# Performance work log

Hardware: AMD Instinct MI355X
Metric: run time of the kernel (lower is better)

The kernel has to match this reference:

```python
import jax, jax.numpy as jnp
import numpy as np
from jax import lax

COCO_80_TO_91 = [1,2,3,4,5,6,7,8,9,10,11,13,14,15,16,17,18,19,20,21,22,23,24,25,27,28,31,32,33,34,35,36,37,38,39,40,41,42,43,44,46,47,48,49,50,51,52,53,54,55,56,57,58,59,60,61,62,63,64,65,67,70,72,73,74,75,76,77,78,79,80,81,82,84,85,86,87,88,89,90]

CONF = 0.25      # self.confidence
IOU_THR = 0.7    # ultralytics NMS default
TOPK = 1000      # candidate cap before NMS
MAX_DET = 300    # ultralytics max_det default
MAX_WH = 7680.0  # per-class offset trick
IMG_SZ = 640.0   # yolov8 letterboxed input size


def setup_inputs() -> dict:
    key = jax.random.key(0)
    preds = jax.random.uniform(key, (32, 84, 8400), dtype=jnp.float32)
    return {"preds": preds}


def _nms_single(boxes, scores):
    """Greedy NMS on score-descending boxes [K,4] (class-offset xyxy). Returns keep mask [K]."""
    K = boxes.shape[0]
    area = (boxes[:, 2] - boxes[:, 0]) * (boxes[:, 3] - boxes[:, 1])  # [K]
    lt = jnp.maximum(boxes[:, None, :2], boxes[None, :, :2])          # [K,K,2]
    rb = jnp.minimum(boxes[:, None, 2:], boxes[None, :, 2:])
    wh = jnp.clip(rb - lt, 0.0)
    inter = wh[..., 0] * wh[..., 1]
    iou = inter / (area[:, None] + area[None, :] - inter + 1e-7)       # [K,K]
    idx = jnp.arange(K)
    sup = (iou > IOU_THR) & (idx[None, :] > idx[:, None])              # i suppresses later j

    def body(i, keep):
        return jnp.where(keep[i], keep & ~sup[i], keep)

    return lax.fori_loop(0, K, body, jnp.ones((K,), dtype=bool))


def reference(preds):
    # preds: [B, 84, N] -> [B, N, 84]
    p = jnp.transpose(preds, (0, 2, 1))
    box_xywh = p[..., :4] * IMG_SZ           # xywh in pixels on 640x640 canvas
    cls = p[..., 4:]                          # [B, N, 80]
    scores = jnp.max(cls, axis=-1)            # best-class confidence
    labels = jnp.argmax(cls, axis=-1)         # 0..79
    xy, wh = box_xywh[..., :2], box_xywh[..., 2:]
    xyxy = jnp.concatenate([xy - wh * 0.5, xy + wh * 0.5], axis=-1)  # decode

    # confidence filter + top-K candidate selection (score-descending)
    s_masked = jnp.where(scores > CONF, scores, -1.0)
    top_s, top_i = lax.top_k(s_masked, TOPK)                          # [B,TOPK]
    top_b = jnp.take_along_axis(xyxy, top_i[..., None], axis=1)      # [B,TOPK,4]
    top_l = jnp.take_along_axis(labels, top_i, axis=1)               # [B,TOPK]

    # per-class NMS via class offset
    off_b = top_b + (top_l.astype(top_b.dtype) * MAX_WH)[..., None]
    keep = jax.vmap(_nms_single)(off_b, top_s) & (top_s > CONF)

    # select final max_det detections, zero-pad invalid slots
    fin_s = jnp.where(keep, top_s, -1.0)
    out_s, out_i = lax.top_k(fin_s, MAX_DET)                          # [B,MAX_DET]
    out_b = jnp.take_along_axis(top_b, out_i[..., None], axis=1)
    out_l = jnp.take_along_axis(top_l, out_i, axis=1)
    valid = out_s > CONF
    boxes = jnp.where(valid[..., None], out_b, 0.0)
    scores_out = jnp.where(valid, out_s, 0.0)
    mapped = jnp.asarray(COCO_80_TO_91, dtype=jnp.int64)[out_l]       # COCO 80 -> 91 ids
    labels_out = jnp.where(valid, mapped, 0)
    return boxes, scores_out, labels_out
```

## Files before the change

kernel.cpp:

```cpp
#include <hip/hip_runtime.h>
#include <stdint.h>

typedef unsigned long long u64;
typedef unsigned int u32;

#define BATCH 32
#define NCH 84
#define NA 8400
#define NCLS 80
#define TOPK 1000
#define MAXDET 300
#define CONF 0.25f
#define IOU_T 0.7f
#define MAX_WH 7680.0f
#define IMG_SZ 640.0f
#define NT 1024
#define KPT 9
#define NCOPY 8
#define HPAD 260

__device__ __constant__ float coco_map_f[NCLS] = {
    1,2,3,4,5,6,7,8,9,10,11,13,14,15,16,17,18,19,20,21,22,23,24,25,27,28,
    31,32,33,34,35,36,37,38,39,40,41,42,43,44,46,47,48,49,50,51,52,53,54,
    55,56,57,58,59,60,61,62,63,64,65,67,70,72,73,74,75,76,77,78,79,80,81,
    82,84,85,86,87,88,89,90};

__device__ inline u64 shflx64(u64 v, int m) {
    int lo = __shfl_xor((int)(u32)(v & 0xFFFFFFFFull), m, 64);
    int hi = __shfl_xor((int)(u32)(v >> 32), m, 64);
    return ((u64)(u32)hi << 32) | (u32)lo;
}

__global__ __launch_bounds__(256)
void decode_kernel(const float* __restrict__ preds,
                   u64* __restrict__ keys,
                   float4* __restrict__ boxes) {
    const int b = blockIdx.y;
    const int a = blockIdx.x * 256 + threadIdx.x;
    const bool live = (a < NA);
    const int ac = live ? a : (NA - 1);
    const float* p = preds + (size_t)b * NCH * NA + ac;

    float bx = p[0];
    float by = p[(size_t)1 * NA];
    float bw = p[(size_t)2 * NA];
    float bh = p[(size_t)3 * NA];

    const float* pc = p + (size_t)4 * NA;
    float best = -1.0f;
    int bl = 0;
#pragma unroll 16
    for (int r = 0; r < NCLS; ++r) {
        float v = pc[(size_t)r * NA];
        bl = (v > best) ? r : bl;
        best = fmaxf(v, best);
    }

    if (live) {
        float fx = bx * IMG_SZ, fy = by * IMG_SZ;
        float fw = bw * IMG_SZ, fh = bh * IMG_SZ;
        float hw = fw * 0.5f, hh = fh * 0.5f;
        boxes[(size_t)b * NA + a] = make_float4(fx - hw, fy - hh, fx + hw, fy + hh);
        float s = (best > CONF) ? best : -1.0f;
        u32 fb = __float_as_uint(s);
        u32 u = (fb & 0x80000000u) ? ~fb : (fb | 0x80000000u);
        keys[(size_t)b * NA + a] =
            ((u64)u << 21) | ((u64)(16383 - a) << 7) | (u64)bl;
    }
}

__global__ __launch_bounds__(NT, 4)
void select_sort_kernel(const u64* __restrict__ keys,
                        const float4* __restrict__ boxes,
                        u64* __restrict__ sortedk,
                        float4* __restrict__ gbox,
                        float4* __restrict__ goffb,
                        float* __restrict__ garea,
                        unsigned short* __restrict__ grank,
                        int* __restrict__ gccnt) {
    const int b = blockIdx.x;
    const int t = threadIdx.x;
    const int lane = t & 63, wid = t >> 6;

    __shared__ union {
        struct {
            u64 sk[2][NT];
            int hist[NCOPY * HPAD];
        } a;
        struct {
            u64 cmask2[NCLS][16];
        } bb;
    } u_s;
    __shared__ int selB, selK, hselS, cnt_s;
    __shared__ int wsum[16], woff[16];

    u64 kreg[KPT];
    const u64* kb = keys + (size_t)b * NA;
#pragma unroll
    for (int j = 0; j < KPT; ++j) {
        int i = t + j * NT;
        kreg[j] = (i < NA) ? kb[i] : 0ull;
    }

    u64 P = 0ull;
    int kk = TOPK;
    int nsel = 0;
    bool done = false;
    bool did16 = false;

    {
        int dg[KPT];
        int mymax = -1;
#pragma unroll
        for (int j = 0; j < KPT; ++j) {
            dg[j] = (kreg[j] != 0ull) ? (int)((kreg[j] >> 37) & 0xFFFF) : -1;
            mymax = max(mymax, dg[j]);
        }
#pragma unroll
        for (int off = 32; off; off >>= 1)
            mymax = max(mymax, __shfl_down(mymax, off, 64));
        if (lane == 0) wsum[wid] = mymax;
        __syncthreads();
        int maxd = wsum[0];
#pragma unroll
        for (int q = 1; q < 16; ++q) maxd = max(maxd, wsum[q]);
        int myc = 0;
#pragma unroll
        for (int j = 0; j < KPT; ++j) myc += (dg[j] == maxd) ? 1 : 0;
#pragma unroll
        for (int off = 32; off; off >>= 1) myc += __shfl_down(myc, off, 64);
        if (lane == 0) woff[wid] = myc;
        __syncthreads();
        int cm = 0;
#pragma unroll
        for (int q = 0; q < 16; ++q) cm += woff[q];
        if (cm >= kk) {
            P = ((u64)maxd) << 37;
            nsel = cm;
            did16 = true;
            done = (nsel <= NT);
        }
    }

    if (!done) {
        const int dstart = did16 ? 1 : 3;
        for (int d = dstart; d >= 0; --d) {
            const int sh = 21 + 8 * d;
            const u64 hmask = (~0ull) << (sh + 8);
            int dig[KPT];
            int mymax = -1;
#pragma unroll
            for (int j = 0; j < KPT; ++j) {
                bool act = (((kreg[j] ^ P) & hmask) == 0ull) && (kreg[j] != 0ull);
                dig[j] = act ? (int)((kreg[j] >> sh) & 255) : -1;
                mymax = max(mymax, dig[j]);
            }
#pragma unroll
            for (int off = 32; off; off >>= 1)
                mymax = max(mymax, __shfl_down(mymax, off, 64));
            if (lane == 0) wsum[wid] = mymax;
            __syncthreads();
            int maxb = wsum[0];
#pragma unroll
            for (int q = 1; q < 16; ++q) maxb = max(maxb, wsum[q]);
            int myc = 0;
#pragma unroll
            for (int j = 0; j < KPT; ++j) myc += (dig[j] == maxb) ? 1 : 0;
#pragma unroll
            for (int off = 32; off; off >>= 1) myc += __shfl_down(myc, off, 64);
            if (lane == 0) woff[wid] = myc;
            __syncthreads();
            int cm = 0;
#pragma unroll
            for (int q = 0; q < 16; ++q) cm += woff[q];
            if (cm >= kk) {
                P |= ((u64)maxb) << sh;
                nsel = TOPK - kk + cm;
                if (nsel <= NT) break;
                continue;
            }
            for (int i = t; i < NCOPY * HPAD; i += NT) u_s.a.hist[i] = 0;
            __syncthreads();
            int* myh = u_s.a.hist + (wid & (NCOPY - 1)) * HPAD;
#pragma unroll
            for (int j = 0; j < KPT; ++j)
                if (dig[j] >= 0) atomicAdd(&myh[dig[j]], 1);
            __syncthreads();
            if (t < 64) {
                int h0 = 0, h1 = 0, h2 = 0, h3 = 0;
                for (int c = 0; c < NCOPY; ++c) {
                    const int* hp = u_s.a.hist + c * HPAD + 4 * t;
                    h0 += hp[0]; h1 += hp[1]; h2 += hp[2]; h3 += hp[3];
                }
                int s = h0 + h1 + h2 + h3;
                int S = s;
                #pragma unroll
                for (int off = 1; off < 64; off <<= 1) {
                    int o = __shfl_down(S, off, 64);
                    if (t + off < 64) S += o;
                }
                int Snext = S - s;
                int c3 = Snext + h3, c2 = c3 + h2, c1 = c2 + h1, c0 = c1 + h0;
                int cand = -1, above = 0;
                if (c0 >= kk) {
                    if      (c3 >= kk) { cand = 4 * t + 3; above = Snext; }
                    else if (c2 >= kk) { cand = 4 * t + 2; above = c3; }
                    else if (c1 >= kk) { cand = 4 * t + 1; above = c2; }
                    else               { cand = 4 * t;     above = c1; }
                }
                int pc = (cand < 0) ? 0 : (((cand + 1) << 16) | (kk - above));
                #pragma unroll
                for (int off = 32; off; off >>= 1)
                    pc = max(pc, __shfl_down(pc, off, 64));
                pc = __shfl(pc, 0, 64);
                int B = (pc >> 16) - 1;
                if (t == (B >> 2)) {
                    int m4 = B & 3;
                    selB = B;
                    selK = pc & 0xFFFF;
                    hselS = (m4 == 0) ? h0 : (m4 == 1) ? h1 : (m4 == 2) ? h2 : h3;
                }
            }
            __syncthreads();
            P |= ((u64)selB) << sh;
            kk = selK;
            nsel = TOPK - kk + hselS;
            if (nsel <= NT) break;
        }
    }

    __syncthreads();
    if (t == 0) cnt_s = 0;
    __syncthreads();
#pragma unroll
    for (int j = 0; j < KPT; ++j) {
        bool p = (kreg[j] >= P);
        u64 m = __ballot(p);
        int base = 0;
        if (lane == 0) base = atomicAdd(&cnt_s, (int)__popcll(m));
        base = __shfl(base, 0, 64);
        if (p) {
            int pos = base + (int)__popcll(m & ((1ull << lane) - 1ull));
            if (pos < NT) u_s.a.sk[0][pos] = kreg[j];
        }
    }
    if (t < NT - nsel) u_s.a.sk[0][nsel + t] = 0ull;
    __syncthreads();

    u64 myk = u_s.a.sk[0][t];
    int buf = 1;
    for (int size = 2; size <= NT; size <<= 1) {
        bool up = ((t & size) == 0);
        for (int stride = size >> 1; stride; stride >>= 1) {
            u64 pk;
            if (stride >= 64) {
                u_s.a.sk[buf][t] = myk;
                __syncthreads();
                pk = u_s.a.sk[buf][t ^ stride];
                buf ^= 1;
            } else {
                pk = shflx64(myk, stride);
            }
            bool tlow = ((t & stride) == 0);
            u64 mn = (myk < pk) ? myk : pk;
            u64 mx = (myk < pk) ? pk : myk;
            myk = up ? (tlow ? mx : mn) : (tlow ? mn : mx);
        }
    }
    sortedk[(size_t)b * NT + t] = myk;

    __syncthreads();
    for (int i = t; i < NCLS * 16; i += NT) ((u64*)u_s.bb.cmask2)[i] = 0ull;
    __syncthreads();

    int my_L = 0;
    float4 bx = make_float4(0.f, 0.f, 0.f, 0.f);
    if (t < TOPK) {
        int my_a = 16383 - (int)((myk >> 7) & 16383ull);
        my_L = (int)(myk & 127ull);
        bx = boxes[(size_t)b * NA + my_a];
        atomicOr(&u_s.bb.cmask2[my_L][t >> 6], 1ull << (t & 63));
    }
    __syncthreads();
    if (t < TOPK) {
        int w = t >> 6;
        int r = __popcll(u_s.bb.cmask2[my_L][w] & ((1ull << (t & 63)) - 1ull));
        for (int q = 0; q < w; ++q) r += __popcll(u_s.bb.cmask2[my_L][q]);
        gbox[(size_t)b * NT + t] = bx;
        if (r < 64) {
            float off = (float)my_L * MAX_WH;
            float ox0 = bx.x + off, oy0 = bx.y + off;
            float ox1 = bx.z + off, oy1 = bx.w + off;
            size_t ci = ((size_t)b * NCLS + my_L) * 64 + r;
            goffb[ci] = make_float4(ox0, oy0, ox1, oy1);
            garea[ci] = (ox1 - ox0) * (oy1 - oy0);
            grank[ci] = (unsigned short)t;
        }
    }
    if (t < NCLS) {
        int s = 0;
#pragma unroll
        for (int q = 0; q < 16; ++q) s += __popcll(u_s.bb.cmask2[t][q]);
        gccnt[(size_t)b * NCLS + t] = s;
    }
}

__global__ __launch_bounds__(NT)
void nms_epi_kernel(const float4* __restrict__ goffb,
                    const float* __restrict__ garea,
                    const unsigned short* __restrict__ grank,
                    const int* __restrict__ gccnt,
                    const u64* __restrict__ sortedk,
                    const float4* __restrict__ gbox,
                    float* __restrict__ out) {
    const int b = blockIdx.x;
    const int t = threadIdx.x;
    const int lane = t & 63, wid = t >> 6;

    __shared__ unsigned char keep[NT];
    __shared__ int wsum[16], woff[16], ktot_s;

    keep[t] = 0;

    int cnts[5];
#pragma unroll
    for (int j = 0; j < 5; ++j)
        cnts[j] = gccnt[(size_t)b * NCLS + wid + 16 * j];

    u64 myk = sortedk[(size_t)b * NT + t];
    __syncthreads();

    for (int j = 0; j < 5; ++j) {
        const int cc = wid + 16 * j;
        const int n = cnts[j];
        if (n == 0) continue;
        if (n <= 64) {
            size_t ci = ((size_t)b * NCLS + cc) * 64 + lane;
            float4 bb = make_float4(0.f, 0.f, 0.f, 0.f);
            float ar = 0.f;
            int rk = 0;
            if (lane < n) { bb = goffb[ci]; ar = garea[ci]; rk = grank[ci]; }
            u64 colm = 0ull;
            for (int i = 0; i < n; ++i) {
                float hx0 = __shfl(bb.x, i, 64);
                float hy0 = __shfl(bb.y, i, 64);
                float hx1 = __shfl(bb.z, i, 64);
                float hy1 = __shfl(bb.w, i, 64);
                float ha  = __shfl(ar, i, 64);
                float lx = fmaxf(hx0, bb.x), ly = fmaxf(hy0, bb.y);
                float rx = fminf(hx1, bb.z), ry = fminf(hy1, bb.w);
                float w = fmaxf(rx - lx, 0.0f);
                float h = fmaxf(ry - ly, 0.0f);
                float inter = w * h;
                float denom = ha + ar;
                denom = denom - inter;
                denom = denom + 1e-7f;
                bool s = (lane > i) && (lane < n) && (inter / denom > IOU_T);
                colm |= ((u64)s) << i;
            }
            u64 alive = (n >= 64) ? ~0ull : ((1ull << n) - 1ull);
            for (int i = 0; i < n; ++i) {
                if (!((alive >> i) & 1ull)) continue;
                alive &= ~__ballot((colm >> i) & 1ull);
            }
            if (lane < n) keep[rk] = (unsigned char)((alive >> lane) & 1ull);
        } else if (lane == 0) {
            const u64* skb = sortedk + (size_t)b * NT;
            const float4* gb = gbox + (size_t)b * NT;
            const float off = (float)cc * MAX_WH;
            u64 aliveW[16];
            for (int q = 0; q < 16; ++q) aliveW[q] = ~0ull;
            for (int i = 0; i < TOPK; ++i) {
                if ((int)(skb[i] & 127ull) != cc) continue;
                if (!((aliveW[i >> 6] >> (i & 63)) & 1ull)) continue;
                float4 g = gb[i];
                float ix0 = g.x + off, iy0 = g.y + off;
                float ix1 = g.z + off, iy1 = g.w + off;
                float ai = (ix1 - ix0) * (iy1 - iy0);
                for (int jj = i + 1; jj < TOPK; ++jj) {
                    if ((int)(skb[jj] & 127ull) != cc) continue;
                    if (!((aliveW[jj >> 6] >> (jj & 63)) & 1ull)) continue;
                    float4 h = gb[jj];
                    float jx0 = h.x + off, jy0 = h.y + off;
                    float jx1 = h.z + off, jy1 = h.w + off;
                    float aj = (jx1 - jx0) * (jy1 - jy0);
                    float lx = fmaxf(ix0, jx0), ly = fmaxf(iy0, jy0);
                    float rx = fminf(ix1, jx1), ry = fminf(iy1, jy1);
                    float ww = fmaxf(rx - lx, 0.0f);
                    float hh = fmaxf(ry - ly, 0.0f);
                    float inter = ww * hh;
                    float denom = ai + aj;
                    denom = denom - inter;
                    denom = denom + 1e-7f;
                    if (inter / denom > IOU_T) aliveW[jj >> 6] &= ~(1ull << (jj & 63));
                }
            }
            for (int i = 0; i < TOPK; ++i)
                if ((int)(skb[i] & 127ull) == cc)
                    keep[i] = (unsigned char)((aliveW[i >> 6] >> (i & 63)) & 1ull);
        }
    }
    __syncthreads();

    float sj = 0.0f;
    bool valid = false;
    if (t < TOPK) {
        u32 u = (u32)(myk >> 21);
        u32 fb = (u & 0x80000000u) ? (u ^ 0x80000000u) : ~u;
        sj = __uint_as_float(fb);
        valid = keep[t] && (sj > CONF);
    }
    u64 m = __ballot(valid);
    if (lane == 0) wsum[wid] = (int)__popcll(m);
    __syncthreads();
    if (wid == 0) {
        int v = (lane < 16) ? wsum[lane] : 0;
        #pragma unroll
        for (int o = 1; o < 16; o <<= 1) {
            int x = __shfl_up(v, o, 64);
            if (lane >= o) v += x;
        }
        if (lane < 16) woff[lane] = v - wsum[lane];
        if (lane == 15) ktot_s = v;
    }
    __syncthreads();
    int ktot = ktot_s;
    int rank = woff[wid] + (int)__popcll(m & ((1ull << lane) - 1ull));

    float* out_boxes = out;
    float* out_scores = out + (size_t)BATCH * MAXDET * 4;
    float* out_labels = out + (size_t)BATCH * MAXDET * 5;
    if (valid && rank < MAXDET) {
        float4 bx = gbox[(size_t)b * NT + t];
        float* ob = out_boxes + ((size_t)b * MAXDET + rank) * 4;
        ob[0] = bx.x; ob[1] = bx.y; ob[2] = bx.z; ob[3] = bx.w;
        out_scores[(size_t)b * MAXDET + rank] = sj;
        out_labels[(size_t)b * MAXDET + rank] = coco_map_f[(int)(myk & 127ull)];
    }
    if (t < MAXDET && t >= ktot) {
        float* ob = out_boxes + ((size_t)b * MAXDET + t) * 4;
        ob[0] = 0.0f; ob[1] = 0.0f; ob[2] = 0.0f; ob[3] = 0.0f;
        out_scores[(size_t)b * MAXDET + t] = 0.0f;
        out_labels[(size_t)b * MAXDET + t] = 0.0f;
    }
}

extern "C" void kernel_launch(void* const* d_in, const int* in_sizes, int n_in,
                              void* d_out, int out_size, void* d_ws, size_t ws_size,
                              hipStream_t stream) {
    const float* preds = (const float*)d_in[0];
    char* ws = (char*)d_ws;
    size_t off = 0;
    auto alloc = [&](size_t bytes) { char* p = ws + off; off += (bytes + 255) & ~(size_t)255; return p; };

    u64* keys            = (u64*)           alloc((size_t)BATCH * NA * 8);
    float4* boxes        = (float4*)        alloc((size_t)BATCH * NA * 16);
    u64* sortedk         = (u64*)           alloc((size_t)BATCH * NT * 8);
    float4* gbox         = (float4*)        alloc((size_t)BATCH * NT * 16);
    float4* goffb        = (float4*)        alloc((size_t)BATCH * NCLS * 64 * 16);
    float* garea         = (float*)         alloc((size_t)BATCH * NCLS * 64 * 4);
    unsigned short* grank= (unsigned short*)alloc((size_t)BATCH * NCLS * 64 * 2);
    int* gccnt           = (int*)           alloc((size_t)BATCH * NCLS * 4);
    float* out = (float*)d_out;

    dim3 dgrid((NA + 255) / 256, BATCH);
    decode_kernel<<<dgrid, 256, 0, stream>>>(preds, keys, boxes);
    select_sort_kernel<<<BATCH, NT, 0, stream>>>(keys, boxes, sortedk, gbox,
                                                 goffb, garea, grank, gccnt);
    nms_epi_kernel<<<BATCH, NT, 0, stream>>>(goffb, garea, grank, gccnt,
                                             sortedk, gbox, out);
}
```

Baseline: 182.2 us.

## Split NMS into a per-class, per-image grid kernel with a separate epilogue

The fused NMS+epilogue kernel, which ran one 1024-thread block per image with each wave handling five classes in turn, is split in two. A new NMS kernel launches one 64-thread block per (class, image) pair and writes keep flags to a global byte buffer. A separate epilogue kernel reads those flags to compact the final detections. The goal is to spread the NMS work over many more compute units instead of only 32 blocks, at the cost of an extra kernel launch and a global round trip for the keep mask.

```diff
diff --git a/kernel.cpp b/kernel.cpp
--- a/kernel.cpp
+++ b/kernel.cpp
@@ -305,110 +305,105 @@
     }
 }
 
+__global__ __launch_bounds__(64)
+void nms_kernel(const float4* __restrict__ goffb,
+                const float* __restrict__ garea,
+                const unsigned short* __restrict__ grank,
+                const int* __restrict__ gccnt,
+                const u64* __restrict__ sortedk,
+                const float4* __restrict__ gbox,
+                unsigned char* __restrict__ keepg) {
+    const int c = blockIdx.x;
+    const int b = blockIdx.y;
+    const int lane = threadIdx.x;
+    const int n = gccnt[(size_t)b * NCLS + c];
+    if (n == 0) return;
+
+    if (n <= 64) {
+        size_t ci = ((size_t)b * NCLS + c) * 64 + lane;
+        float4 bb = make_float4(0.f, 0.f, 0.f, 0.f);
+        float ar = 0.f;
+        int rk = 0;
+        if (lane < n) { bb = goffb[ci]; ar = garea[ci]; rk = grank[ci]; }
+        u64 colm = 0ull;
+        for (int i = 0; i < n; ++i) {
+            float hx0 = __shfl(bb.x, i, 64);
+            float hy0 = __shfl(bb.y, i, 64);
+            float hx1 = __shfl(bb.z, i, 64);
+            float hy1 = __shfl(bb.w, i, 64);
+            float ha  = __shfl(ar, i, 64);
+            float lx = fmaxf(hx0, bb.x), ly = fmaxf(hy0, bb.y);
+            float rx = fminf(hx1, bb.z), ry = fminf(hy1, bb.w);
+            float w = fmaxf(rx - lx, 0.0f);
+            float h = fmaxf(ry - ly, 0.0f);
+            float inter = w * h;
+            float denom = ha + ar;
+            denom = denom - inter;
+            denom = denom + 1e-7f;
+            bool s = (lane > i) && (lane < n) && (inter / denom > IOU_T);
+            colm |= ((u64)s) << i;
+        }
+        u64 alive = (n >= 64) ? ~0ull : ((1ull << n) - 1ull);
+        for (int i = 0; i < n; ++i) {
+            if (!((alive >> i) & 1ull)) continue;
+            alive &= ~__ballot((colm >> i) & 1ull);
+        }
+        if (lane < n) keepg[(size_t)b * NT + rk] = (unsigned char)((alive >> lane) & 1ull);
+    } else if (lane == 0) {
+        const u64* skb = sortedk + (size_t)b * NT;
+        const float4* gb = gbox + (size_t)b * NT;
+        const float off = (float)c * MAX_WH;
+        u64 aliveW[16];
+        for (int q = 0; q < 16; ++q) aliveW[q] = ~0ull;
+        for (int i = 0; i < TOPK; ++i) {
+            if ((int)(skb[i] & 127ull) != c) continue;
+            if (!((aliveW[i >> 6] >> (i & 63)) & 1ull)) continue;
+            float4 g = gb[i];
+            float ix0 = g.x + off, iy0 = g.y + off;
+            float ix1 = g.z + off, iy1 = g.w + off;
+            float ai = (ix1 - ix0) * (iy1 - iy0);
+            for (int jj = i + 1; jj < TOPK; ++jj) {
+                if ((int)(skb[jj] & 127ull) != c) continue;
+                if (!((aliveW[jj >> 6] >> (jj & 63)) & 1ull)) continue;
+                float4 h = gb[jj];
+                float jx0 = h.x + off, jy0 = h.y + off;
+                float jx1 = h.z + off, jy1 = h.w + off;
+                float aj = (jx1 - jx0) * (jy1 - jy0);
+                float lx = fmaxf(ix0, jx0), ly = fmaxf(iy0, jy0);
+                float rx = fminf(ix1, jx1), ry = fminf(iy1, jy1);
+                float ww = fmaxf(rx - lx, 0.0f);
+                float hh = fmaxf(ry - ly, 0.0f);
+                float inter = ww * hh;
+                float denom = ai + aj;
+                denom = denom - inter;
+                denom = denom + 1e-7f;
+                if (inter / denom > IOU_T) aliveW[jj >> 6] &= ~(1ull << (jj & 63));
+            }
+        }
+        for (int i = 0; i < TOPK; ++i)
+            if ((int)(skb[i] & 127ull) == c)
+                keepg[(size_t)b * NT + i] = (unsigned char)((aliveW[i >> 6] >> (i & 63)) & 1ull);
+    }
+}
+
 __global__ __launch_bounds__(NT)
-void nms_epi_kernel(const float4* __restrict__ goffb,
-                    const float* __restrict__ garea,
-                    const unsigned short* __restrict__ grank,
-                    const int* __restrict__ gccnt,
-                    const u64* __restrict__ sortedk,
-                    const float4* __restrict__ gbox,
-                    float* __restrict__ out) {
+void epilogue_kernel(const u64* __restrict__ sortedk,
+                     const unsigned char* __restrict__ keepg,
+                     const float4* __restrict__ gbox,
+                     float* __restrict__ out) {
     const int b = blockIdx.x;
     const int t = threadIdx.x;
     const int lane = t & 63, wid = t >> 6;
-
-    __shared__ unsigned char keep[NT];
     __shared__ int wsum[16], woff[16], ktot_s;
 
-    keep[t] = 0;
-
-    int cnts[5];
-#pragma unroll
-    for (int j = 0; j < 5; ++j)
-        cnts[j] = gccnt[(size_t)b * NCLS + wid + 16 * j];
-
     u64 myk = sortedk[(size_t)b * NT + t];
-    __syncthreads();
-
-    for (int j = 0; j < 5; ++j) {
-        const int cc = wid + 16 * j;
-        const int n = cnts[j];
-        if (n == 0) continue;
-        if (n <= 64) {
-            size_t ci = ((size_t)b * NCLS + cc) * 64 + lane;
-            float4 bb = make_float4(0.f, 0.f, 0.f, 0.f);
-            float ar = 0.f;
-            int rk = 0;
-            if (lane < n) { bb = goffb[ci]; ar = garea[ci]; rk = grank[ci]; }
-            u64 colm = 0ull;
-            for (int i = 0; i < n; ++i) {
-                float hx0 = __shfl(bb.x, i, 64);
-                float hy0 = __shfl(bb.y, i, 64);
-                float hx1 = __shfl(bb.z, i, 64);
-                float hy1 = __shfl(bb.w, i, 64);
-                float ha  = __shfl(ar, i, 64);
-                float lx = fmaxf(hx0, bb.x), ly = fmaxf(hy0, bb.y);
-                float rx = fminf(hx1, bb.z), ry = fminf(hy1, bb.w);
-                float w = fmaxf(rx - lx, 0.0f);
-                float h = fmaxf(ry - ly, 0.0f);
-                float inter = w * h;
-                float denom = ha + ar;
-                denom = denom - inter;
-                denom = denom + 1e-7f;
-                bool s = (lane > i) && (lane < n) && (inter / denom > IOU_T);
-                colm |= ((u64)s) << i;
-            }
-            u64 alive = (n >= 64) ? ~0ull : ((1ull << n) - 1ull);
-            for (int i = 0; i < n; ++i) {
-                if (!((alive >> i) & 1ull)) continue;
-                alive &= ~__ballot((colm >> i) & 1ull);
-            }
-            if (lane < n) keep[rk] = (unsigned char)((alive >> lane) & 1ull);
-        } else if (lane == 0) {
-            const u64* skb = sortedk + (size_t)b * NT;
-            const float4* gb = gbox + (size_t)b * NT;
-            const float off = (float)cc * MAX_WH;
-            u64 aliveW[16];
-            for (int q = 0; q < 16; ++q) aliveW[q] = ~0ull;
-            for (int i = 0; i < TOPK; ++i) {
-                if ((int)(skb[i] & 127ull) != cc) continue;
-                if (!((aliveW[i >> 6] >> (i & 63)) & 1ull)) continue;
-                float4 g = gb[i];
-                float ix0 = g.x + off, iy0 = g.y + off;
-                float ix1 = g.z + off, iy1 = g.w + off;
-                float ai = (ix1 - ix0) * (iy1 - iy0);
-                for (int jj = i + 1; jj < TOPK; ++jj) {
-                    if ((int)(skb[jj] & 127ull) != cc) continue;
-                    if (!((aliveW[jj >> 6] >> (jj & 63)) & 1ull)) continue;
-                    float4 h = gb[jj];
-                    float jx0 = h.x + off, jy0 = h.y + off;
-                    float jx1 = h.z + off, jy1 = h.w + off;
-                    float aj = (jx1 - jx0) * (jy1 - jy0);
-                    float lx = fmaxf(ix0, jx0), ly = fmaxf(iy0, jy0);
-                    float rx = fminf(ix1, jx1), ry = fminf(iy1, jy1);
-                    float ww = fmaxf(rx - lx, 0.0f);
-                    float hh = fmaxf(ry - ly, 0.0f);
-                    float inter = ww * hh;
-                    float denom = ai + aj;
-                    denom = denom - inter;
-                    denom = denom + 1e-7f;
-                    if (inter / denom > IOU_T) aliveW[jj >> 6] &= ~(1ull << (jj & 63));
-                }
-            }
-            for (int i = 0; i < TOPK; ++i)
-                if ((int)(skb[i] & 127ull) == cc)
-                    keep[i] = (unsigned char)((aliveW[i >> 6] >> (i & 63)) & 1ull);
-        }
-    }
-    __syncthreads();
-
+    bool valid = false;
     float sj = 0.0f;
-    bool valid = false;
     if (t < TOPK) {
         u32 u = (u32)(myk >> 21);
         u32 fb = (u & 0x80000000u) ? (u ^ 0x80000000u) : ~u;
         sj = __uint_as_float(fb);
-        valid = keep[t] && (sj > CONF);
+        valid = keepg[(size_t)b * NT + t] && (sj > CONF);
     }
     u64 m = __ballot(valid);
     if (lane == 0) wsum[wid] = (int)__popcll(m);
@@ -416,9 +411,9 @@
     if (wid == 0) {
         int v = (lane < 16) ? wsum[lane] : 0;
         #pragma unroll
-        for (int o = 1; o < 16; o <<= 1) {
-            int x = __shfl_up(v, o, 64);
-            if (lane >= o) v += x;
+        for (int off = 1; off < 16; off <<= 1) {
+            int o = __shfl_up(v, off, 64);
+            if (lane >= off) v += o;
         }
         if (lane < 16) woff[lane] = v - wsum[lane];
         if (lane == 15) ktot_s = v;
@@ -461,12 +456,15 @@
     float* garea         = (float*)         alloc((size_t)BATCH * NCLS * 64 * 4);
     unsigned short* grank= (unsigned short*)alloc((size_t)BATCH * NCLS * 64 * 2);
     int* gccnt           = (int*)           alloc((size_t)BATCH * NCLS * 4);
+    unsigned char* keepg = (unsigned char*) alloc((size_t)BATCH * NT);
     float* out = (float*)d_out;
 
     dim3 dgrid((NA + 255) / 256, BATCH);
     decode_kernel<<<dgrid, 256, 0, stream>>>(preds, keys, boxes);
     select_sort_kernel<<<BATCH, NT, 0, stream>>>(keys, boxes, sortedk, gbox,
                                                  goffb, garea, grank, gccnt);
-    nms_epi_kernel<<<BATCH, NT, 0, stream>>>(goffb, garea, grank, gccnt,
-                                             sortedk, gbox, out);
-}
+    dim3 ngrid(NCLS, BATCH);
+    nms_kernel<<<ngrid, 64, 0, stream>>>(goffb, garea, grank, gccnt,
+                                         sortedk, gbox, keepg);
+    epilogue_kernel<<<BATCH, NT, 0, stream>>>(sortedk, keepg, gbox, out);
+}
```

Result: faster. 163.2 us (-10.4%).
